# Kernel optimization log

Measured on AMD Instinct MI355X. Metric: run time of the kernel, lower is better.

## Reference

```python
import jax, jax.numpy as jnp
import numpy as np

N = 1_000_000   # total stacked points across the batch
D = 256         # feature dim
B = 16          # number of clouds (segments)


def setup_inputs() -> dict:
    key = jax.random.key(0)
    kx, ks = jax.random.split(key)
    x = jax.random.normal(kx, (N, D), dtype=jnp.float32)
    # sorted segment ids <=> contiguous ragged batch segments (i0:i0+length slices)
    segment_ids = jnp.sort(jax.random.randint(ks, (N,), 0, B, dtype=jnp.int32))
    return {"x": x, "segment_ids": segment_ids}


def reference(x, segment_ids):
    # Fused segment-mean: one scatter-add pass over x instead of a Python
    # loop of per-segment torch.mean calls.
    sums = jax.ops.segment_sum(x, segment_ids, num_segments=B)            # [B, D]
    counts = jax.ops.segment_sum(jnp.ones((x.shape[0],), x.dtype),
                                 segment_ids, num_segments=B)             # [B]
    return sums / jnp.maximum(counts, 1.0)[:, None]                      # [B, D]
```

## Files before the change

kernel.cpp:

```cpp
#include <hip/hip_runtime.h>


constexpr int D = 256;
constexpr int B = 16;

__global__ void zero_ws_kernel(float* __restrict__ ws, int n) {
    int i = blockIdx.x * blockDim.x + threadIdx.x;
    if (i < n) ws[i] = 0.0f;
}

__device__ __forceinline__ void flush_acc(int cur, const float4& acc, int cnt,
                                          int lane, float* __restrict__ sums,
                                          float* __restrict__ counts) {
    if (cur < 0 || cnt == 0) return;
    float* p = sums + cur * D + lane * 4;
    atomicAdd(p + 0, acc.x);
    atomicAdd(p + 1, acc.y);
    atomicAdd(p + 2, acc.z);
    atomicAdd(p + 3, acc.w);
    if (lane == 0) atomicAdd(counts + cur, (float)cnt);
}

__global__ __launch_bounds__(256) void seg_sum_kernel(
        const float4* __restrict__ x, const int* __restrict__ seg,
        float* __restrict__ sums, float* __restrict__ counts, int N) {
    const int lane = threadIdx.x & 63;
    const int wave = threadIdx.x >> 6;

    const int rowsPerBlock = (N + gridDim.x - 1) / gridDim.x;
    const int r0 = blockIdx.x * rowsPerBlock;
    const int r1 = min(N, r0 + rowsPerBlock);

    float4 acc = make_float4(0.f, 0.f, 0.f, 0.f);
    int cur = -1;
    int cnt = 0;

    for (int r = r0 + wave; r < r1; r += 4) {
        int s = seg[r];
        float4 v = x[(long long)r * (D / 4) + lane];
        if (s != cur) {
            flush_acc(cur, acc, cnt, lane, sums, counts);
            acc = make_float4(0.f, 0.f, 0.f, 0.f);
            cnt = 0;
            cur = s;
        }
        acc.x += v.x; acc.y += v.y; acc.z += v.z; acc.w += v.w;
        ++cnt;
    }
    flush_acc(cur, acc, cnt, lane, sums, counts);
}

__global__ void finalize_kernel(const float* __restrict__ sums,
                                const float* __restrict__ counts,
                                float* __restrict__ out) {
    int i = blockIdx.x * blockDim.x + threadIdx.x;
    if (i < B * D) {
        int b = i >> 8;
        out[i] = sums[i] / fmaxf(counts[b], 1.0f);
    }
}

extern "C" void kernel_launch(void* const* d_in, const int* in_sizes, int n_in,
                              void* d_out, int out_size, void* d_ws, size_t ws_size,
                              hipStream_t stream) {
    const float4* x  = (const float4*)d_in[0];
    const int*   seg = (const int*)d_in[1];
    float*       out = (float*)d_out;

    const int N = in_sizes[1];

    float* sums   = (float*)d_ws;
    float* counts = sums + B * D;
    const int nws = B * D + B;
    zero_ws_kernel<<<(nws + 255) / 256, 256, 0, stream>>>(sums, nws);

    const int blocks = 1024;
    seg_sum_kernel<<<blocks, 256, 0, stream>>>(x, seg, sums, counts, N);

    finalize_kernel<<<(B * D + 255) / 256, 256, 0, stream>>>(sums, counts, out);
}
```

Before: 227.7 us.

## Use grid-stride LDS-privatized segment sums with per-block partials and a separate reduce

Replaces the chunked global-atomic segment sum with a 512-thread grid-stride kernel. Each block accumulates per-segment sums in shared memory and writes a private partial row, and a second kernel reduces the partials and divides by the counts. The main loop issues four row loads per iteration to keep more memory requests in flight, and the zero-init kernel is dropped. The cost is an extra partial buffer of several MB written and re-read, plus a fallback path if the workspace is too small.

```diff
diff --git a/kernel.cpp b/kernel.cpp
--- a/kernel.cpp
+++ b/kernel.cpp
@@ -4,14 +4,115 @@
 constexpr int D = 256;
 constexpr int B = 16;
 
+constexpr int TPB         = 512;
+constexpr int MAIN_BLOCKS = 512;
+constexpr int WPB         = TPB / 64;
+constexpr int RS          = MAIN_BLOCKS * WPB;
+constexpr int PART_STRIDE = B * D + B;
+
+
+__device__ __forceinline__ void lds_flush(float* __restrict__ lsum,
+                                          int* __restrict__ lcnt,
+                                          int cur, const float4& acc, int cnt,
+                                          int lane) {
+    if (cur < 0 || cnt == 0) return;
+    float* p = lsum + cur * D + lane * 4;
+    atomicAdd(p + 0, acc.x);
+    atomicAdd(p + 1, acc.y);
+    atomicAdd(p + 2, acc.z);
+    atomicAdd(p + 3, acc.w);
+    if (lane == 0) atomicAdd(lcnt + cur, cnt);
+}
+
+__device__ __forceinline__ void step(float* __restrict__ lsum,
+                                     int* __restrict__ lcnt, int lane,
+                                     int s, const float4& v,
+                                     int& cur, float4& acc, int& cnt) {
+    if (s != cur) {
+        lds_flush(lsum, lcnt, cur, acc, cnt, lane);
+        cur = s; acc = v; cnt = 1;
+    } else {
+        acc.x += v.x; acc.y += v.y; acc.z += v.z; acc.w += v.w;
+        ++cnt;
+    }
+}
+
+__global__ __launch_bounds__(TPB) void seg_sum_stride(
+        const float4* __restrict__ x, const int* __restrict__ seg,
+        float* __restrict__ part, int N) {
+    __shared__ float lsum[B * D];
+    __shared__ int   lcnt[B];
+
+    const int t = threadIdx.x;
+    for (int i = t; i < B * D; i += TPB) lsum[i] = 0.f;
+    if (t < B) lcnt[t] = 0;
+    __syncthreads();
+
+    const int lane = t & 63;
+    const int wave = t >> 6;
+    const int gwid = blockIdx.x * WPB + wave;
+
+    float4 acc = make_float4(0.f, 0.f, 0.f, 0.f);
+    int cur = -1, cnt = 0;
+
+    int r = gwid;
+    for (; r + 3 * RS < N; r += 4 * RS) {
+        const int s0 = seg[r];
+        const int s3 = seg[r + 3 * RS];
+        float4 v0 = x[(size_t)r            * (D / 4) + lane];
+        float4 v1 = x[(size_t)(r +     RS) * (D / 4) + lane];
+        float4 v2 = x[(size_t)(r + 2 * RS) * (D / 4) + lane];
+        float4 v3 = x[(size_t)(r + 3 * RS) * (D / 4) + lane];
+        if (s0 == cur && s3 == cur) {
+            acc.x += v0.x + v1.x + v2.x + v3.x;
+            acc.y += v0.y + v1.y + v2.y + v3.y;
+            acc.z += v0.z + v1.z + v2.z + v3.z;
+            acc.w += v0.w + v1.w + v2.w + v3.w;
+            cnt += 4;
+        } else {
+            const int s1 = seg[r + RS], s2 = seg[r + 2 * RS];
+            step(lsum, lcnt, lane, s0, v0, cur, acc, cnt);
+            step(lsum, lcnt, lane, s1, v1, cur, acc, cnt);
+            step(lsum, lcnt, lane, s2, v2, cur, acc, cnt);
+            step(lsum, lcnt, lane, s3, v3, cur, acc, cnt);
+        }
+    }
+    for (; r < N; r += RS) {
+        const int s = seg[r];
+        float4 v = x[(size_t)r * (D / 4) + lane];
+        step(lsum, lcnt, lane, s, v, cur, acc, cnt);
+    }
+    lds_flush(lsum, lcnt, cur, acc, cnt, lane);
+    __syncthreads();
+
+    float* dst = part + (size_t)blockIdx.x * PART_STRIDE;
+    for (int i = t; i < B * D; i += TPB) dst[i] = lsum[i];
+    if (t < B) dst[B * D + t] = (float)lcnt[t];
+}
+
+__global__ void reduce_part(const float* __restrict__ part,
+                            float* __restrict__ out) {
+    const int i = blockIdx.x * blockDim.x + threadIdx.x;
+    if (i >= B * D) return;
+    const int s = i >> 8;
+    float ssum = 0.f, csum = 0.f;
+#pragma unroll 4
+    for (int b = 0; b < MAIN_BLOCKS; ++b) {
+        ssum += part[(size_t)b * PART_STRIDE + i];
+        csum += part[(size_t)b * PART_STRIDE + B * D + s];
+    }
+    out[i] = ssum / fmaxf(csum, 1.f);
+}
+
+
 __global__ void zero_ws_kernel(float* __restrict__ ws, int n) {
     int i = blockIdx.x * blockDim.x + threadIdx.x;
     if (i < n) ws[i] = 0.0f;
 }
 
-__device__ __forceinline__ void flush_acc(int cur, const float4& acc, int cnt,
-                                          int lane, float* __restrict__ sums,
-                                          float* __restrict__ counts) {
+__device__ __forceinline__ void flush_acc_wave(int cur, const float4& acc, int cnt,
+                                               int lane, float* __restrict__ sums,
+                                               float* __restrict__ counts) {
     if (cur < 0 || cnt == 0) return;
     float* p = sums + cur * D + lane * 4;
     atomicAdd(p + 0, acc.x);
@@ -21,25 +122,22 @@
     if (lane == 0) atomicAdd(counts + cur, (float)cnt);
 }
 
-__global__ __launch_bounds__(256) void seg_sum_kernel(
+__global__ __launch_bounds__(256) void seg_sum_chunked(
         const float4* __restrict__ x, const int* __restrict__ seg,
         float* __restrict__ sums, float* __restrict__ counts, int N) {
     const int lane = threadIdx.x & 63;
     const int wave = threadIdx.x >> 6;
-
     const int rowsPerBlock = (N + gridDim.x - 1) / gridDim.x;
     const int r0 = blockIdx.x * rowsPerBlock;
     const int r1 = min(N, r0 + rowsPerBlock);
-
+    if (r0 >= r1) return;
     float4 acc = make_float4(0.f, 0.f, 0.f, 0.f);
-    int cur = -1;
-    int cnt = 0;
-
+    int cur = -1, cnt = 0;
     for (int r = r0 + wave; r < r1; r += 4) {
         int s = seg[r];
-        float4 v = x[(long long)r * (D / 4) + lane];
+        float4 v = x[(size_t)r * (D / 4) + lane];
         if (s != cur) {
-            flush_acc(cur, acc, cnt, lane, sums, counts);
+            flush_acc_wave(cur, acc, cnt, lane, sums, counts);
             acc = make_float4(0.f, 0.f, 0.f, 0.f);
             cnt = 0;
             cur = s;
@@ -47,7 +145,7 @@
         acc.x += v.x; acc.y += v.y; acc.z += v.z; acc.w += v.w;
         ++cnt;
     }
-    flush_acc(cur, acc, cnt, lane, sums, counts);
+    flush_acc_wave(cur, acc, cnt, lane, sums, counts);
 }
 
 __global__ void finalize_kernel(const float* __restrict__ sums,
@@ -60,22 +158,26 @@
     }
 }
 
+
 extern "C" void kernel_launch(void* const* d_in, const int* in_sizes, int n_in,
                               void* d_out, int out_size, void* d_ws, size_t ws_size,
                               hipStream_t stream) {
     const float4* x  = (const float4*)d_in[0];
     const int*   seg = (const int*)d_in[1];
     float*       out = (float*)d_out;
-
     const int N = in_sizes[1];
 
-    float* sums   = (float*)d_ws;
-    float* counts = sums + B * D;
-    const int nws = B * D + B;
-    zero_ws_kernel<<<(nws + 255) / 256, 256, 0, stream>>>(sums, nws);
-
-    const int blocks = 1024;
-    seg_sum_kernel<<<blocks, 256, 0, stream>>>(x, seg, sums, counts, N);
-
-    finalize_kernel<<<(B * D + 255) / 256, 256, 0, stream>>>(sums, counts, out);
+    const size_t need = (size_t)MAIN_BLOCKS * PART_STRIDE * sizeof(float);
+    if (ws_size >= need) {
+        float* part = (float*)d_ws;
+        seg_sum_stride<<<MAIN_BLOCKS, TPB, 0, stream>>>(x, seg, part, N);
+        reduce_part<<<(B * D + 63) / 64, 64, 0, stream>>>(part, out);
+    } else {
+        float* sums   = (float*)d_ws;
+        float* counts = sums + B * D;
+        const int nws = B * D + B;
+        zero_ws_kernel<<<(nws + 255) / 256, 256, 0, stream>>>(sums, nws);
+        seg_sum_chunked<<<1024, 256, 0, stream>>>(x, seg, sums, counts, N);
+        finalize_kernel<<<(B * D + 255) / 256, 256, 0, stream>>>(sums, counts, out);
+    }
 }
```

Result: slower. 240.8 us (+5.8%).
